# Kernel tuning notes

Measured on AMD Instinct MI355X. Metric: run time of the kernel, lower is better.

Reference implementation:

```python
import jax, jax.numpy as jnp
import numpy as np

TEMPERATURE = 0.02


def setup_inputs() -> dict:
    key = jax.random.key(0)
    kq, kp = jax.random.split(key)
    query_embeddings = jax.random.normal(kq, (32, 32, 128), dtype=jnp.float32)      # [b, s, h]
    positive_embeddings = jax.random.normal(kp, (512, 128, 128), dtype=jnp.float32)  # [c, d, h]
    return {"query_embeddings": query_embeddings, "positive_embeddings": positive_embeddings}


def reference(query_embeddings, positive_embeddings):
    # Late interaction: all query tokens vs all doc tokens across the (in-)batch.
    # [b, c, s, d]
    late = jnp.einsum('bsh,cdh->bcsd', query_embeddings, positive_embeddings)
    # MaxSim: max over doc tokens, sum over query tokens -> [b, c]
    scores = late.max(axis=-1).sum(axis=-1) / TEMPERATURE
    # CrossEntropyLoss(reduction='mean') with labels = zeros(b)
    loss = jnp.mean(jax.nn.logsumexp(scores, axis=-1) - scores[:, 0])
    return loss
```

## Files before the change

kernel.cpp:

```cpp
#include <hip/hip_runtime.h>

#define BQ 32
#define H  128
#define C  512
#define D  128

typedef _Float16 half8v __attribute__((ext_vector_type(8)));
typedef float floatx16 __attribute__((ext_vector_type(16)));

__global__ __launch_bounds__(256) void qprep_kernel(const float* __restrict__ q,
                                                    _Float16* __restrict__ qs,
                                                    float* __restrict__ out) {
  int t = blockIdx.x * 256 + threadIdx.x;
  if (t == 0) out[0] = 0.0f;
  int lane = t & 63;
  int kb   = (t >> 6) & 7;
  int b    = t >> 9;
  int s    = lane & 31;
  int h    = kb * 16 + (lane >> 5) * 8;
  const float* src = q + ((b * 32 + s) * H + h);
  float4 v0 = *(const float4*)src;
  float4 v1 = *(const float4*)(src + 4);
  half8v o = { (_Float16)v0.x, (_Float16)v0.y, (_Float16)v0.z, (_Float16)v0.w,
               (_Float16)v1.x, (_Float16)v1.y, (_Float16)v1.z, (_Float16)v1.w };
  *(half8v*)(qs + (size_t)t * 8) = o;
}

__global__ __launch_bounds__(256, 2) void scores_kernel(const float* __restrict__ pos,
                                                        const _Float16* __restrict__ qs,
                                                        float* __restrict__ scores) {
  const int c    = blockIdx.x;
  const int tid  = threadIdx.x;
  const int w    = tid >> 6;
  const int lane = tid & 63;
  const int mrow = lane & 31;
  const int khi  = (lane >> 5) * 8;

  __shared__ float pmm[BQ][4][32];

  const half8v* qf = (const half8v*)qs;
  const float*  pc = pos + (size_t)c * (D * H);

  half8v   pa[8];
  half8v   qb[3][8];
  floatx16 acc[2];

  floatx16 zc;
#pragma unroll
  for (int i = 0; i < 16; ++i) zc[i] = 0.0f;

#pragma unroll
  for (int kb = 0; kb < 8; ++kb) {
    const float* src = pc + ((w * 32 + mrow) * H + kb * 16 + khi);
    float4 v0 = *(const float4*)src;
    float4 v1 = *(const float4*)(src + 4);
    half8v f = { (_Float16)v0.x, (_Float16)v0.y, (_Float16)v0.z, (_Float16)v0.w,
                 (_Float16)v1.x, (_Float16)v1.y, (_Float16)v1.z, (_Float16)v1.w };
    pa[kb] = f;
  }

#pragma unroll
  for (int kb = 0; kb < 8; ++kb) qb[0][kb] = qf[kb * 64 + lane];
#pragma unroll
  for (int kb = 0; kb < 8; ++kb) qb[1][kb] = qf[(8 + kb) * 64 + lane];

  auto reduce_store = [&](int b, floatx16& a) {
    float m01 = fmaxf(fmaxf(a[0],  a[1]),  fmaxf(a[2],  a[3]));
    float m23 = fmaxf(fmaxf(a[4],  a[5]),  fmaxf(a[6],  a[7]));
    float m45 = fmaxf(fmaxf(a[8],  a[9]),  fmaxf(a[10], a[11]));
    float m67 = fmaxf(fmaxf(a[12], a[13]), fmaxf(a[14], a[15]));
    float m = fmaxf(fmaxf(m01, m23), fmaxf(m45, m67));
    m = fmaxf(m, __shfl_xor(m, 32));
    if (lane < 32) pmm[b][w][lane] = m;
  };

  acc[0] = __builtin_amdgcn_mfma_f32_32x32x16_f16(pa[0], qb[0][0], zc, 0, 0, 0);
#pragma unroll
  for (int kb = 1; kb < 8; ++kb)
    acc[0] = __builtin_amdgcn_mfma_f32_32x32x16_f16(pa[kb], qb[0][kb], acc[0], 0, 0, 0);

#pragma unroll
  for (int b = 1; b < BQ; ++b) {
    const int cur = b & 1, prv = cur ^ 1;
    if (b + 1 < BQ) {
      const int nb = (b + 1) * 8;
      half8v* dst = qb[(b + 1) % 3];
#pragma unroll
      for (int kb = 0; kb < 8; ++kb) dst[kb] = qf[(nb + kb) * 64 + lane];
    }
    const half8v* qc = qb[b % 3];
    acc[cur] = __builtin_amdgcn_mfma_f32_32x32x16_f16(pa[0], qc[0], zc, 0, 0, 0);
#pragma unroll
    for (int kb = 1; kb < 8; ++kb)
      acc[cur] = __builtin_amdgcn_mfma_f32_32x32x16_f16(pa[kb], qc[kb], acc[cur], 0, 0, 0);
    reduce_store(b - 1, acc[prv]);
  }
  reduce_store(BQ - 1, acc[1]);

  __syncthreads();

  {
    int b  = tid >> 3;
    int sq = tid & 7;
    float4 x0 = *(float4*)&pmm[b][0][sq * 4];
    float4 x1 = *(float4*)&pmm[b][1][sq * 4];
    float4 x2 = *(float4*)&pmm[b][2][sq * 4];
    float4 x3 = *(float4*)&pmm[b][3][sq * 4];
    float mx_x = fmaxf(fmaxf(x0.x, x1.x), fmaxf(x2.x, x3.x));
    float mx_y = fmaxf(fmaxf(x0.y, x1.y), fmaxf(x2.y, x3.y));
    float mx_z = fmaxf(fmaxf(x0.z, x1.z), fmaxf(x2.z, x3.z));
    float mx_w = fmaxf(fmaxf(x0.w, x1.w), fmaxf(x2.w, x3.w));
    float v = (mx_x + mx_y) + (mx_z + mx_w);
    v += __shfl_xor(v, 1);
    v += __shfl_xor(v, 2);
    v += __shfl_xor(v, 4);
    if (sq == 0) scores[b * C + c] = v * 50.0f;
  }
}

__global__ __launch_bounds__(256) void loss_kernel(const float* __restrict__ scores,
                                                   float* __restrict__ out) {
  __shared__ float red[8];
  const int b = blockIdx.x, tid = threadIdx.x, w = tid >> 6, lane = tid & 63;
  const float* row = scores + b * C;
  float x0 = row[tid], x1 = row[tid + 256];
  float mx = fmaxf(x0, x1);
#pragma unroll
  for (int off = 1; off < 64; off <<= 1) mx = fmaxf(mx, __shfl_xor(mx, off));
  if (lane == 0) red[w] = mx;
  __syncthreads();
  float bmax = fmaxf(fmaxf(red[0], red[1]), fmaxf(red[2], red[3]));
  float e = __expf(x0 - bmax) + __expf(x1 - bmax);
#pragma unroll
  for (int off = 1; off < 64; off <<= 1) e += __shfl_xor(e, off);
  if (lane == 0) red[4 + w] = e;
  __syncthreads();
  if (tid == 0) {
    float s = red[4] + red[5] + red[6] + red[7];
    atomicAdd(out, (bmax + __logf(s) - row[0]) * (1.0f / 32.0f));
  }
}

extern "C" void kernel_launch(void* const* d_in, const int* in_sizes, int n_in,
                              void* d_out, int out_size, void* d_ws, size_t ws_size,
                              hipStream_t stream) {
  const float* q = (const float*)d_in[0];
  const float* p = (const float*)d_in[1];
  float* scores  = (float*)d_ws;
  _Float16* qs   = (_Float16*)((char*)d_ws + 65536);

  qprep_kernel<<<64, 256, 0, stream>>>(q, qs, (float*)d_out);
  scores_kernel<<<C, 256, 0, stream>>>(p, qs, scores);
  loss_kernel<<<32, 256, 0, stream>>>(scores, (float*)d_out);
}
```

Baseline: 96.42 us.

## Use two waves per block each covering two 32-row doc tiles to reuse query fragments

The scores kernel now runs 128 threads (2 waves) per block, and each wave computes two 32-row M tiles of doc tokens against the same query B fragments. Query fragment loads per block are halved and each load feeds twice as many MFMAs, while the cross-wave shared-memory reduction shrinks from four to two partials. In exchange each wave holds double the A operands and accumulators (higher VGPR pressure), and there are fewer waves per block to hide memory latency.

```diff
diff --git a/kernel.cpp b/kernel.cpp
--- a/kernel.cpp
+++ b/kernel.cpp
@@ -26,7 +26,7 @@
   *(half8v*)(qs + (size_t)t * 8) = o;
 }
 
-__global__ __launch_bounds__(256, 2) void scores_kernel(const float* __restrict__ pos,
+__global__ __launch_bounds__(128, 1) void scores_kernel(const float* __restrict__ pos,
                                                         const _Float16* __restrict__ qs,
                                                         float* __restrict__ scores) {
   const int c    = blockIdx.x;
@@ -36,48 +36,59 @@
   const int mrow = lane & 31;
   const int khi  = (lane >> 5) * 8;
 
-  __shared__ float pmm[BQ][4][32];
+  __shared__ float pmm[BQ][2][32];
 
   const half8v* qf = (const half8v*)qs;
   const float*  pc = pos + (size_t)c * (D * H);
 
-  half8v   pa[8];
+  half8v   pa[2][8];
   half8v   qb[3][8];
-  floatx16 acc[2];
+  floatx16 acc[2][2];
 
   floatx16 zc;
 #pragma unroll
   for (int i = 0; i < 16; ++i) zc[i] = 0.0f;
 
 #pragma unroll
-  for (int kb = 0; kb < 8; ++kb) {
-    const float* src = pc + ((w * 32 + mrow) * H + kb * 16 + khi);
-    float4 v0 = *(const float4*)src;
-    float4 v1 = *(const float4*)(src + 4);
-    half8v f = { (_Float16)v0.x, (_Float16)v0.y, (_Float16)v0.z, (_Float16)v0.w,
-                 (_Float16)v1.x, (_Float16)v1.y, (_Float16)v1.z, (_Float16)v1.w };
-    pa[kb] = f;
-  }
+  for (int kb = 0; kb < 8; ++kb)
+#pragma unroll
+    for (int mt = 0; mt < 2; ++mt) {
+      const float* src = pc + ((w * 64 + mt * 32 + mrow) * H + kb * 16 + khi);
+      float4 v0 = *(const float4*)src;
+      float4 v1 = *(const float4*)(src + 4);
+      half8v f = { (_Float16)v0.x, (_Float16)v0.y, (_Float16)v0.z, (_Float16)v0.w,
+                   (_Float16)v1.x, (_Float16)v1.y, (_Float16)v1.z, (_Float16)v1.w };
+      pa[mt][kb] = f;
+    }
 
 #pragma unroll
   for (int kb = 0; kb < 8; ++kb) qb[0][kb] = qf[kb * 64 + lane];
 #pragma unroll
   for (int kb = 0; kb < 8; ++kb) qb[1][kb] = qf[(8 + kb) * 64 + lane];
 
-  auto reduce_store = [&](int b, floatx16& a) {
-    float m01 = fmaxf(fmaxf(a[0],  a[1]),  fmaxf(a[2],  a[3]));
-    float m23 = fmaxf(fmaxf(a[4],  a[5]),  fmaxf(a[6],  a[7]));
-    float m45 = fmaxf(fmaxf(a[8],  a[9]),  fmaxf(a[10], a[11]));
-    float m67 = fmaxf(fmaxf(a[12], a[13]), fmaxf(a[14], a[15]));
-    float m = fmaxf(fmaxf(m01, m23), fmaxf(m45, m67));
+  auto reduce_store = [&](int b, floatx16 (&a)[2]) {
+    float m0 = fmaxf(fmaxf(a[0][0],  a[0][1]),  fmaxf(a[0][2],  a[0][3]));
+    float m1 = fmaxf(fmaxf(a[0][4],  a[0][5]),  fmaxf(a[0][6],  a[0][7]));
+    float m2 = fmaxf(fmaxf(a[0][8],  a[0][9]),  fmaxf(a[0][10], a[0][11]));
+    float m3 = fmaxf(fmaxf(a[0][12], a[0][13]), fmaxf(a[0][14], a[0][15]));
+    float n0 = fmaxf(fmaxf(a[1][0],  a[1][1]),  fmaxf(a[1][2],  a[1][3]));
+    float n1 = fmaxf(fmaxf(a[1][4],  a[1][5]),  fmaxf(a[1][6],  a[1][7]));
+    float n2 = fmaxf(fmaxf(a[1][8],  a[1][9]),  fmaxf(a[1][10], a[1][11]));
+    float n3 = fmaxf(fmaxf(a[1][12], a[1][13]), fmaxf(a[1][14], a[1][15]));
+    float m = fmaxf(fmaxf(fmaxf(m0, m1), fmaxf(m2, m3)),
+                    fmaxf(fmaxf(n0, n1), fmaxf(n2, n3)));
     m = fmaxf(m, __shfl_xor(m, 32));
     if (lane < 32) pmm[b][w][lane] = m;
   };
 
-  acc[0] = __builtin_amdgcn_mfma_f32_32x32x16_f16(pa[0], qb[0][0], zc, 0, 0, 0);
+#pragma unroll
+  for (int mt = 0; mt < 2; ++mt)
+    acc[0][mt] = __builtin_amdgcn_mfma_f32_32x32x16_f16(pa[mt][0], qb[0][0], zc, 0, 0, 0);
 #pragma unroll
   for (int kb = 1; kb < 8; ++kb)
-    acc[0] = __builtin_amdgcn_mfma_f32_32x32x16_f16(pa[kb], qb[0][kb], acc[0], 0, 0, 0);
+#pragma unroll
+    for (int mt = 0; mt < 2; ++mt)
+      acc[0][mt] = __builtin_amdgcn_mfma_f32_32x32x16_f16(pa[mt][kb], qb[0][kb], acc[0][mt], 0, 0, 0);
 
 #pragma unroll
   for (int b = 1; b < BQ; ++b) {
@@ -89,10 +100,14 @@
       for (int kb = 0; kb < 8; ++kb) dst[kb] = qf[(nb + kb) * 64 + lane];
     }
     const half8v* qc = qb[b % 3];
-    acc[cur] = __builtin_amdgcn_mfma_f32_32x32x16_f16(pa[0], qc[0], zc, 0, 0, 0);
+#pragma unroll
+    for (int mt = 0; mt < 2; ++mt)
+      acc[cur][mt] = __builtin_amdgcn_mfma_f32_32x32x16_f16(pa[mt][0], qc[0], zc, 0, 0, 0);
 #pragma unroll
     for (int kb = 1; kb < 8; ++kb)
-      acc[cur] = __builtin_amdgcn_mfma_f32_32x32x16_f16(pa[kb], qc[kb], acc[cur], 0, 0, 0);
+#pragma unroll
+      for (int mt = 0; mt < 2; ++mt)
+        acc[cur][mt] = __builtin_amdgcn_mfma_f32_32x32x16_f16(pa[mt][kb], qc[kb], acc[cur][mt], 0, 0, 0);
     reduce_store(b - 1, acc[prv]);
   }
   reduce_store(BQ - 1, acc[1]);
@@ -100,20 +115,15 @@
   __syncthreads();
 
   {
-    int b  = tid >> 3;
-    int sq = tid & 7;
-    float4 x0 = *(float4*)&pmm[b][0][sq * 4];
-    float4 x1 = *(float4*)&pmm[b][1][sq * 4];
-    float4 x2 = *(float4*)&pmm[b][2][sq * 4];
-    float4 x3 = *(float4*)&pmm[b][3][sq * 4];
-    float mx_x = fmaxf(fmaxf(x0.x, x1.x), fmaxf(x2.x, x3.x));
-    float mx_y = fmaxf(fmaxf(x0.y, x1.y), fmaxf(x2.y, x3.y));
-    float mx_z = fmaxf(fmaxf(x0.z, x1.z), fmaxf(x2.z, x3.z));
-    float mx_w = fmaxf(fmaxf(x0.w, x1.w), fmaxf(x2.w, x3.w));
-    float v = (mx_x + mx_y) + (mx_z + mx_w);
+    int b  = tid >> 2;
+    int sq = tid & 3;
+    const float* p0 = &pmm[b][0][sq * 8];
+    const float* p1 = &pmm[b][1][sq * 8];
+    float v = 0.f;
+#pragma unroll
+    for (int j = 0; j < 8; ++j) v += fmaxf(p0[j], p1[j]);
     v += __shfl_xor(v, 1);
     v += __shfl_xor(v, 2);
-    v += __shfl_xor(v, 4);
     if (sq == 0) scores[b * C + c] = v * 50.0f;
   }
 }
@@ -150,6 +160,6 @@
   _Float16* qs   = (_Float16*)((char*)d_ws + 65536);
 
   qprep_kernel<<<64, 256, 0, stream>>>(q, qs, (float*)d_out);
-  scores_kernel<<<C, 256, 0, stream>>>(p, qs, scores);
+  scores_kernel<<<C, 128, 0, stream>>>(p, qs, scores);
   loss_kernel<<<32, 256, 0, stream>>>(scores, (float*)d_out);
 }
```

After: 99.81 us. +3.5%, slower.
